# Optimization experiments

Measured on AMD Instinct MI355X. Metric: run time of the kernel, lower is better.

## Reference

```python
import jax, jax.numpy as jnp
import numpy as np

B, T, EMB, H = 4, 2048, 1024, 16
S = EMB // H


def setup_inputs() -> dict:
    key = jax.random.key(0)
    ks = jax.random.split(key, 7)
    x = jax.random.normal(ks[0], (B, T, EMB), dtype=jnp.float32)
    pad_amounts = jax.random.randint(ks[1], (B,), 0, 512, dtype=jnp.int64)
    Wk = jax.random.normal(ks[2], (S, S), dtype=jnp.float32) * (1.0 / np.sqrt(S))
    Wq = jax.random.normal(ks[3], (S, S), dtype=jnp.float32) * (1.0 / np.sqrt(S))
    Wv = jax.random.normal(ks[4], (S, S), dtype=jnp.float32) * (1.0 / np.sqrt(S))
    Wu = jax.random.normal(ks[5], (EMB, EMB), dtype=jnp.float32) * (1.0 / np.sqrt(EMB))
    bu = jax.random.normal(ks[6], (EMB,), dtype=jnp.float32) * 0.01
    return {"x": x, "Wk": Wk, "Wq": Wq, "Wv": Wv, "Wu": Wu, "bu": bu,
            "pad_amounts": pad_amounts}


def reference(x, Wk, Wq, Wv, Wu, bu, pad_amounts):
    b, t, e = x.shape
    h = H
    s = e // h
    xh = x.reshape(b, t, h, s)
    # torch Linear: y = x @ W.T (no bias for k/q/v)
    keys = jnp.einsum('bths,os->btho', xh, Wk)
    queries = jnp.einsum('bths,os->btho', xh, Wq)
    values = jnp.einsum('bths,os->btho', xh, Wv)
    # (b,t,h,s) -> (b*h,t,s)
    keys = keys.transpose(0, 2, 1, 3).reshape(b * h, t, s)
    queries = queries.transpose(0, 2, 1, 3).reshape(b * h, t, s)
    values = values.transpose(0, 2, 1, 3).reshape(b * h, t, s)
    scale = e ** 0.25
    queries = queries / scale
    keys = keys / scale
    dot = jnp.einsum('nqs,nks->nqk', queries, keys)  # (b*h, t, t)
    # Faithful to original bug: only the first b flat indices of b*h get masked.
    pad_full = jnp.concatenate([pad_amounts,
                                jnp.zeros(b * h - b, dtype=pad_amounts.dtype)])
    thresh = (t - pad_full)[:, None, None]  # (b*h,1,1); thresh=t -> no mask
    pos = jnp.arange(t)
    mask = (pos[None, :, None] >= thresh) & (pos[None, None, :] >= thresh)
    dot = jnp.where(mask, -jnp.inf, dot)
    att = jax.nn.softmax(dot, axis=2)
    out = jnp.einsum('nqk,nks->nqs', att, values)  # (b*h,t,s)
    out = out.reshape(b, h, t, s).transpose(0, 2, 1, 3).reshape(b, t, h * s)
    return out @ Wu.T + bu
```

## Files before the change

### kernel.cpp

```cpp
#include <hip/hip_runtime.h>


typedef float f32x4 __attribute__((ext_vector_type(4)));
typedef float f32x16 __attribute__((ext_vector_type(16)));
typedef _Float16 f16x2 __attribute__((ext_vector_type(2)));
typedef _Float16 f16x8 __attribute__((ext_vector_type(8)));
typedef unsigned u32x4 __attribute__((ext_vector_type(4)));

#define MFMA16(a, b, c) __builtin_amdgcn_mfma_f32_16x16x32_f16((a), (b), (c), 0, 0, 0)
#define MFMA32(a, b, c) __builtin_amdgcn_mfma_f32_32x32x16_f16((a), (b), (c), 0, 0, 0)

constexpr int Tn = 2048;
constexpr int Bn = 4;
constexpr int EMBn = 1024;
constexpr float NEG_INF = -3.0e38f;

__device__ __forceinline__ float exp2_hw(float x) {
  float r; asm("v_exp_f32 %0, %1" : "=v"(r) : "v"(x)); return r;
}
__device__ __forceinline__ unsigned pkrtz(float lo, float hi) {
  unsigned r; asm("v_cvt_pkrtz_f16_f32 %0, %1, %2" : "=v"(r) : "v"(lo), "v"(hi)); return r;
}
__device__ __forceinline__ unsigned pkadd(unsigned a, unsigned b) {
  unsigned r; asm("v_pk_add_f16 %0, %1, %2" : "=v"(r) : "v"(a), "v"(b)); return r;
}
__device__ __forceinline__ void permswap(unsigned& a, unsigned& b) {
  asm("v_permlane32_swap_b32 %0, %1" : "+v"(a), "+v"(b));
}

__global__ __launch_bounds__(256) void sa_prep(
    const float* __restrict__ Wk, const float* __restrict__ Wq,
    const float* __restrict__ Wv, const float* __restrict__ Wu,
    _Float16* __restrict__ w3, _Float16* __restrict__ wub) {
  int idx = blockIdx.x * 256 + threadIdx.x;
  const float rs = 0.21233046f;
  if (idx < 1048576) wub[idx] = (_Float16)Wu[idx];
  if (idx < 4096) {
    w3[idx]        = (_Float16)(Wk[idx] * rs);
    w3[4096 + idx] = (_Float16)(Wq[idx] * rs);
    w3[8192 + idx] = (_Float16)(Wv[idx]);
  }
}

__global__ __launch_bounds__(256) void sa_qkv(
    const float* __restrict__ x, const _Float16* __restrict__ w3,
    _Float16* __restrict__ Qb, _Float16* __restrict__ Kb, _Float16* __restrict__ Vt) {
  const int wave = threadIdx.x >> 6;
  const int lane = threadIdx.x & 63;
  const int g = lane >> 4, c = lane & 15;
  const int n = blockIdx.y, b = n >> 4, h = n & 15;
  const int t0 = blockIdx.x * 64 + wave * 16;

  f16x8 ax[2];
#pragma unroll
  for (int kk = 0; kk < 2; ++kk) {
    const float* xp = x + ((long)((b * Tn + t0 + c) * 16 + h)) * 64 + kk * 32 + g * 8;
    f32x4 u = *(const f32x4*)xp;
    f32x4 v = *(const f32x4*)(xp + 4);
    f16x8 a;
    a[0] = (_Float16)u[0]; a[1] = (_Float16)u[1]; a[2] = (_Float16)u[2]; a[3] = (_Float16)u[3];
    a[4] = (_Float16)v[0]; a[5] = (_Float16)v[1]; a[6] = (_Float16)v[2]; a[7] = (_Float16)v[3];
    ax[kk] = a;
  }

#pragma unroll
  for (int w = 0; w < 2; ++w) {
    _Float16* dst = w ? Qb : Kb;
#pragma unroll
    for (int ot = 0; ot < 4; ++ot) {
      f32x4 a_ = {0.f, 0.f, 0.f, 0.f};
#pragma unroll
      for (int kk = 0; kk < 2; ++kk) {
        f16x8 wf = *(const f16x8*)(w3 + w * 4096 + (ot * 16 + c) * 64 + kk * 32 + g * 8);
        a_ = MFMA16(ax[kk], wf, a_);
      }
#pragma unroll
      for (int r = 0; r < 4; ++r)
        dst[((long)n * Tn + t0 + g * 4 + r) * 64 + ot * 16 + c] = (_Float16)a_[r];
    }
  }

#pragma unroll
  for (int ot = 0; ot < 4; ++ot) {
    f32x4 a_ = {0.f, 0.f, 0.f, 0.f};
#pragma unroll
    for (int kk = 0; kk < 2; ++kk) {
      f16x8 wf = *(const f16x8*)(w3 + 8192 + (ot * 16 + c) * 64 + kk * 32 + g * 8);
      a_ = MFMA16(wf, ax[kk], a_);
    }
#pragma unroll
    for (int r = 0; r < 4; ++r)
      Vt[((long)n * 64 + ot * 16 + g * 4 + r) * Tn + t0 + c] = (_Float16)a_[r];
  }
}

__global__ __launch_bounds__(256, 4) void sa_flash(
    const _Float16* __restrict__ Qb, const _Float16* __restrict__ Kb,
    const _Float16* __restrict__ Vt, const int* __restrict__ pad32,
    _Float16* __restrict__ AO) {
  const int bid = blockIdx.x;
  const int n = (bid & 7) * 8 + (bid >> 7);
  const int qblk = (bid >> 3) & 15;
  const int tid = threadIdx.x;
  const int wave = tid >> 6;
  const int lane = tid & 63;
  const int ql = lane & 31;
  const int hi = lane >> 5;

  int thresh = Tn;
  if (n < Bn) {
    bool is64 = (pad32[1] == 0 && pad32[3] == 0);
    int pv = is64 ? pad32[2 * n] : pad32[n];
    thresh = Tn - pv;
  }

  const int qbase = qblk * 128 + wave * 32;
  const _Float16* Qh = Qb + (long)n * Tn * 64;
  const _Float16* Kh = Kb + (long)n * Tn * 64;
  const _Float16* Vh = Vt + (long)n * 64 * Tn;

  f16x8 bq[4];
  const _Float16* qp = Qh + (long)(qbase + ql) * 64 + hi * 8;
#pragma unroll
  for (int ks = 0; ks < 4; ++ks) bq[ks] = *(const f16x8*)(qp + ks * 16);

  __shared__ __align__(16) char smem[36864];

  const int sr = tid >> 2, sc = tid & 3;
  const _Float16* kgp = Kh + sr * 64 + sc * 8;
  const _Float16* vgp = Vh + (long)sr * Tn + sc * 8;
  char* kw = smem + sr * 144 + sc * 16;
  char* vw = smem + 18432 + sr * 144 + sc * 16;

  f32x16 o[2];
  f32x16 zf;
#pragma unroll
  for (int i = 0; i < 16; ++i) { o[0][i] = 0.f; o[1][i] = 0.f; zf[i] = 0.f; }
  float l = 0.f;

  const bool qge = (qbase + ql) >= thresh;
  const bool qany = (qbase + 32) > thresh;

  {
    f16x8 k0 = *(const f16x8*)kgp;
    f16x8 k1 = *(const f16x8*)(kgp + 32);
    f16x8 v0 = *(const f16x8*)vgp;
    f16x8 v1 = *(const f16x8*)(vgp + 32);
    *(f16x8*)kw = k0;
    *(f16x8*)(kw + 64) = k1;
    *(f16x8*)vw = v0;
    *(f16x8*)(vw + 64) = v1;
  }
  __syncthreads();

  int cur = 0;
  for (int kb = 0; kb < Tn; kb += 64) {
    const int kbn = (kb + 64) & (Tn - 1);
    f16x8 kst0 = *(const f16x8*)(kgp + kbn * 64);
    f16x8 kst1 = *(const f16x8*)(kgp + kbn * 64 + 32);
    f16x8 vst0 = *(const f16x8*)(vgp + kbn);
    f16x8 vst1 = *(const f16x8*)(vgp + kbn + 32);

    const char* kbb = smem + cur * 9216;
    const char* vbb = smem + 18432 + cur * 9216;

#pragma unroll
    for (int sub = 0; sub < 2; ++sub) {
      const char* krow = kbb + (sub * 32 + ql) * 144 + hi * 16;
      f16x8 ka0 = *(const f16x8*)(krow);
      f16x8 ka1 = *(const f16x8*)(krow + 32);
      f16x8 ka2 = *(const f16x8*)(krow + 64);
      f16x8 ka3 = *(const f16x8*)(krow + 96);

      __builtin_amdgcn_s_setprio(1);
      f32x16 st = MFMA32(ka0, bq[0], zf);
      st = MFMA32(ka1, bq[1], st);
      st = MFMA32(ka2, bq[2], st);
      st = MFMA32(ka3, bq[3], st);
      __builtin_amdgcn_s_setprio(0);

      if (qany && (kb + sub * 32 + 32) > thresh) {
        if (qge) {
#pragma unroll
          for (int r = 0; r < 16; ++r) {
            int kr_ = kb + sub * 32 + (r & 3) + 8 * (r >> 2) + 4 * hi;
            if (kr_ >= thresh) st[r] = NEG_INF;
          }
        }
      }

      float p[16];
#pragma unroll
      for (int r = 0; r < 16; ++r) p[r] = exp2_hw(st[r]);

      unsigned pw[8], psum[2];
#pragma unroll
      for (int j = 0; j < 2; ++j) {
        unsigned a0 = pkrtz(p[j * 8 + 0], p[j * 8 + 1]);
        unsigned b0 = pkrtz(p[j * 8 + 4], p[j * 8 + 5]);
        unsigned a1 = pkrtz(p[j * 8 + 2], p[j * 8 + 3]);
        unsigned b1 = pkrtz(p[j * 8 + 6], p[j * 8 + 7]);
        psum[j] = pkadd(pkadd(a0, b0), pkadd(a1, b1));
        permswap(a0, b0);
        permswap(a1, b1);
        pw[j * 4 + 0] = a0; pw[j * 4 + 1] = a1;
        pw[j * 4 + 2] = b0; pw[j * 4 + 3] = b1;
      }
      {
        f16x2 ph = __builtin_bit_cast(f16x2, pkadd(psum[0], psum[1]));
        l += (float)ph[0] + (float)ph[1];
      }
      u32x4 u0 = {pw[0], pw[1], pw[2], pw[3]};
      u32x4 u1 = {pw[4], pw[5], pw[6], pw[7]};
      f16x8 pb0 = __builtin_bit_cast(f16x8, u0);
      f16x8 pb1 = __builtin_bit_cast(f16x8, u1);

      const char* vrow0 = vbb + ql * 144 + sub * 64 + hi * 16;
      const char* vrow1 = vrow0 + 32 * 144;
      f16x8 va0 = *(const f16x8*)(vrow0);
      f16x8 va1 = *(const f16x8*)(vrow0 + 32);
      f16x8 va2 = *(const f16x8*)(vrow1);
      f16x8 va3 = *(const f16x8*)(vrow1 + 32);

      __builtin_amdgcn_s_setprio(1);
      o[0] = MFMA32(va0, pb0, o[0]);
      o[0] = MFMA32(va1, pb1, o[0]);
      o[1] = MFMA32(va2, pb0, o[1]);
      o[1] = MFMA32(va3, pb1, o[1]);
      __builtin_amdgcn_s_setprio(0);
    }

    char* kwd = kw + (cur ^ 1) * 9216;
    char* vwd = vw + (cur ^ 1) * 9216;
    *(f16x8*)kwd = kst0;
    *(f16x8*)(kwd + 64) = kst1;
    *(f16x8*)vwd = vst0;
    *(f16x8*)(vwd + 64) = vst1;
    __syncthreads();
    cur ^= 1;
  }

  float lf = l + __shfl_xor(l, 32, 64);
  float linv = 1.0f / lf;

  _Float16* my = (_Float16*)(smem + wave * 4096);
#pragma unroll
  for (int stile = 0; stile < 2; ++stile) {
#pragma unroll
    for (int r = 0; r < 16; r += 2) {
      unsigned wv = pkrtz(o[stile][r] * linv, o[stile][r + 1] * linv);
      int s = stile * 32 + (r & 3) + 8 * (r >> 2) + 4 * hi;
      *(unsigned*)(my + ql * 64 + (s ^ ((ql & 7) << 3))) = wv;
    }
  }
  asm volatile("s_waitcnt lgkmcnt(0)" ::: "memory");

  const int bb = n >> 4, hh = n & 15;
  const int qr = lane >> 3, s0 = (lane & 7) * 8;
#pragma unroll
  for (int j = 0; j < 4; ++j) {
    int q = j * 8 + qr;
    f16x8 vv = *(const f16x8*)(my + q * 64 + (s0 ^ ((q & 7) << 3)));
    *(f16x8*)(AO + ((long)(bb * Tn + qbase + q)) * EMBn + hh * 64 + s0) = vv;
  }
}

__global__ __launch_bounds__(256, 4) void sa_oproj(
    const _Float16* __restrict__ A, const _Float16* __restrict__ WuB,
    const float* __restrict__ bu, float* __restrict__ Y) {
  const int bid = blockIdx.x;
  const int xcd = bid & 7;
  const int j = bid >> 3;
  const int nstrip = j & 15;
  const int mblk = xcd * 8 + (j >> 4);
  const int tid = threadIdx.x;
  const int wave = tid >> 6;
  const int lane = tid & 63;
  const int ql = lane & 31;
  const int hi = lane >> 5;
  const int mbase = mblk * 128 + wave * 32;
  const int nbase = nstrip * 64;

  __shared__ __align__(16) char bsm[18432];
  const int sr = tid >> 3, sc = tid & 7;
  const _Float16* wg0 = WuB + (long)(nbase + sr) * 1024 + sc * 8;
  const _Float16* wg1 = WuB + (long)(nbase + sr + 32) * 1024 + sc * 8;
  char* ww0 = bsm + sr * 144 + sc * 16;
  char* ww1 = bsm + (sr + 32) * 144 + sc * 16;

  const _Float16* ap = A + (long)(mbase + ql) * 1024 + hi * 8;

  f32x16 acc[2];
#pragma unroll
  for (int i = 0; i < 16; ++i) { acc[0][i] = 0.f; acc[1][i] = 0.f; }

  {
    f16x8 w0 = *(const f16x8*)wg0;
    f16x8 w1 = *(const f16x8*)wg1;
    *(f16x8*)ww0 = w0;
    *(f16x8*)ww1 = w1;
  }
  __syncthreads();

  int cur = 0;
  for (int kb = 0; kb < 1024; kb += 64) {
    const int kbn = (kb + 64) & 1023;
    f16x8 wn0 = *(const f16x8*)(wg0 + kbn);
    f16x8 wn1 = *(const f16x8*)(wg1 + kbn);

    f16x8 af[4];
#pragma unroll
    for (int ks = 0; ks < 4; ++ks) af[ks] = *(const f16x8*)(ap + kb + ks * 16);

    const char* bbase = bsm + cur * 9216;
#pragma unroll
    for (int nt = 0; nt < 2; ++nt) {
      const char* brow = bbase + (nt * 32 + ql) * 144;
#pragma unroll
      for (int ks = 0; ks < 4; ++ks) {
        f16x8 bf = *(const f16x8*)(brow + (ks * 2 + hi) * 16);
        acc[nt] = MFMA32(af[ks], bf, acc[nt]);
      }
    }

    *(f16x8*)(ww0 + (cur ^ 1) * 9216) = wn0;
    *(f16x8*)(ww1 + (cur ^ 1) * 9216) = wn1;
    __syncthreads();
    cur ^= 1;
  }

#pragma unroll
  for (int nt = 0; nt < 2; ++nt) {
    float bias = bu[nbase + nt * 32 + ql];
#pragma unroll
    for (int r = 0; r < 16; ++r) {
      int mrow = mbase + (r & 3) + 8 * (r >> 2) + 4 * hi;
      Y[(long)mrow * 1024 + nbase + nt * 32 + ql] = acc[nt][r] + bias;
    }
  }
}

extern "C" void kernel_launch(void* const* d_in, const int* in_sizes, int n_in,
                              void* d_out, int out_size, void* d_ws, size_t ws_size,
                              hipStream_t stream) {
  const float* x  = (const float*)d_in[0];
  const float* Wk = (const float*)d_in[1];
  const float* Wq = (const float*)d_in[2];
  const float* Wv = (const float*)d_in[3];
  const float* Wu = (const float*)d_in[4];
  const float* bu = (const float*)d_in[5];
  const int* pad  = (const int*)d_in[6];
  float* Y = (float*)d_out;

  _Float16* ws  = (_Float16*)d_ws;
  _Float16* w3  = ws;
  _Float16* wub = ws + 16384;
  _Float16* Qb  = ws + 16384 + 1048576;
  _Float16* Kb  = Qb + 8388608;
  _Float16* Vt  = Kb + 8388608;
  _Float16* AO  = Vt + 8388608;

  sa_prep<<<4096, 256, 0, stream>>>(Wk, Wq, Wv, Wu, w3, wub);
  sa_qkv<<<dim3(32, 64), 256, 0, stream>>>(x, w3, Qb, Kb, Vt);
  sa_flash<<<dim3(1024), 256, 0, stream>>>(Qb, Kb, Vt, pad, AO);
  sa_oproj<<<dim3(1024), 256, 0, stream>>>(AO, wub, bu, Y);
}
```

Before: 153.0 us.

## Fuse Wu fp16 conversion into out-projection and split QK/softmax phases

Removes the separate pass that converts the 1024x1024 Wu matrix to fp16 in the prep kernel. The out-projection kernel now loads fp32 Wu tiles and converts them to fp16 in registers before writing to LDS, and the prep launch shrinks to 16 blocks. Separately, the flash kernel computes both 32-row QK^T sub-tiles before running exp/softmax on either, to give the scheduler more independent MFMA work. The cost is twice the global bytes for Wu reads in oproj, repeated across blocks, plus higher register pressure in the flash loop.

```diff
diff --git a/kernel.cpp b/kernel.cpp
--- a/kernel.cpp
+++ b/kernel.cpp
@@ -30,11 +30,9 @@
 
 __global__ __launch_bounds__(256) void sa_prep(
     const float* __restrict__ Wk, const float* __restrict__ Wq,
-    const float* __restrict__ Wv, const float* __restrict__ Wu,
-    _Float16* __restrict__ w3, _Float16* __restrict__ wub) {
+    const float* __restrict__ Wv, _Float16* __restrict__ w3) {
   int idx = blockIdx.x * 256 + threadIdx.x;
   const float rs = 0.21233046f;
-  if (idx < 1048576) wub[idx] = (_Float16)Wu[idx];
   if (idx < 4096) {
     w3[idx]        = (_Float16)(Wk[idx] * rs);
     w3[4096 + idx] = (_Float16)(Wq[idx] * rs);
@@ -164,6 +162,7 @@
     const char* kbb = smem + cur * 9216;
     const char* vbb = smem + 18432 + cur * 9216;
 
+    f32x16 st[2];
 #pragma unroll
     for (int sub = 0; sub < 2; ++sub) {
       const char* krow = kbb + (sub * 32 + ql) * 144 + hi * 16;
@@ -171,12 +170,11 @@
       f16x8 ka1 = *(const f16x8*)(krow + 32);
       f16x8 ka2 = *(const f16x8*)(krow + 64);
       f16x8 ka3 = *(const f16x8*)(krow + 96);
-
       __builtin_amdgcn_s_setprio(1);
-      f32x16 st = MFMA32(ka0, bq[0], zf);
-      st = MFMA32(ka1, bq[1], st);
-      st = MFMA32(ka2, bq[2], st);
-      st = MFMA32(ka3, bq[3], st);
+      f32x16 s_ = MFMA32(ka0, bq[0], zf);
+      s_ = MFMA32(ka1, bq[1], s_);
+      s_ = MFMA32(ka2, bq[2], s_);
+      s_ = MFMA32(ka3, bq[3], s_);
       __builtin_amdgcn_s_setprio(0);
 
       if (qany && (kb + sub * 32 + 32) > thresh) {
@@ -184,14 +182,18 @@
 #pragma unroll
           for (int r = 0; r < 16; ++r) {
             int kr_ = kb + sub * 32 + (r & 3) + 8 * (r >> 2) + 4 * hi;
-            if (kr_ >= thresh) st[r] = NEG_INF;
+            if (kr_ >= thresh) s_[r] = NEG_INF;
           }
         }
       }
-
+      st[sub] = s_;
+    }
+
+#pragma unroll
+    for (int sub = 0; sub < 2; ++sub) {
       float p[16];
 #pragma unroll
-      for (int r = 0; r < 16; ++r) p[r] = exp2_hw(st[r]);
+      for (int r = 0; r < 16; ++r) p[r] = exp2_hw(st[sub][r]);
 
       unsigned pw[8], psum[2];
 #pragma unroll
@@ -266,7 +268,7 @@
 }
 
 __global__ __launch_bounds__(256, 4) void sa_oproj(
-    const _Float16* __restrict__ A, const _Float16* __restrict__ WuB,
+    const _Float16* __restrict__ A, const float* __restrict__ Wu,
     const float* __restrict__ bu, float* __restrict__ Y) {
   const int bid = blockIdx.x;
   const int xcd = bid & 7;
@@ -283,8 +285,8 @@
 
   __shared__ __align__(16) char bsm[18432];
   const int sr = tid >> 3, sc = tid & 7;
-  const _Float16* wg0 = WuB + (long)(nbase + sr) * 1024 + sc * 8;
-  const _Float16* wg1 = WuB + (long)(nbase + sr + 32) * 1024 + sc * 8;
+  const float* wg0 = Wu + (long)(nbase + sr) * 1024 + sc * 8;
+  const float* wg1 = Wu + (long)(nbase + sr + 32) * 1024 + sc * 8;
   char* ww0 = bsm + sr * 144 + sc * 16;
   char* ww1 = bsm + (sr + 32) * 144 + sc * 16;
 
@@ -294,9 +296,21 @@
 #pragma unroll
   for (int i = 0; i < 16; ++i) { acc[0][i] = 0.f; acc[1][i] = 0.f; }
 
+  auto cvt8 = [](const float* p) -> f16x8 {
+    f32x4 a = *(const f32x4*)p;
+    f32x4 b = *(const f32x4*)(p + 4);
+    unsigned r0, r1, r2, r3;
+    asm("v_cvt_pkrtz_f16_f32 %0, %1, %2" : "=v"(r0) : "v"(a[0]), "v"(a[1]));
+    asm("v_cvt_pkrtz_f16_f32 %0, %1, %2" : "=v"(r1) : "v"(a[2]), "v"(a[3]));
+    asm("v_cvt_pkrtz_f16_f32 %0, %1, %2" : "=v"(r2) : "v"(b[0]), "v"(b[1]));
+    asm("v_cvt_pkrtz_f16_f32 %0, %1, %2" : "=v"(r3) : "v"(b[2]), "v"(b[3]));
+    u32x4 u = {r0, r1, r2, r3};
+    return __builtin_bit_cast(f16x8, u);
+  };
+
   {
-    f16x8 w0 = *(const f16x8*)wg0;
-    f16x8 w1 = *(const f16x8*)wg1;
+    f16x8 w0 = cvt8(wg0);
+    f16x8 w1 = cvt8(wg1);
     *(f16x8*)ww0 = w0;
     *(f16x8*)ww1 = w1;
   }
@@ -305,8 +319,8 @@
   int cur = 0;
   for (int kb = 0; kb < 1024; kb += 64) {
     const int kbn = (kb + 64) & 1023;
-    f16x8 wn0 = *(const f16x8*)(wg0 + kbn);
-    f16x8 wn1 = *(const f16x8*)(wg1 + kbn);
+    f16x8 wn0 = cvt8(wg0 + kbn);
+    f16x8 wn1 = cvt8(wg1 + kbn);
 
     f16x8 af[4];
 #pragma unroll
@@ -354,14 +368,13 @@
 
   _Float16* ws  = (_Float16*)d_ws;
   _Float16* w3  = ws;
-  _Float16* wub = ws + 16384;
-  _Float16* Qb  = ws + 16384 + 1048576;
+  _Float16* Qb  = ws + 16384;
   _Float16* Kb  = Qb + 8388608;
   _Float16* Vt  = Kb + 8388608;
   _Float16* AO  = Vt + 8388608;
 
-  sa_prep<<<4096, 256, 0, stream>>>(Wk, Wq, Wv, Wu, w3, wub);
+  sa_prep<<<16, 256, 0, stream>>>(Wk, Wq, Wv, w3);
   sa_qkv<<<dim3(32, 64), 256, 0, stream>>>(x, w3, Qb, Kb, Vt);
   sa_flash<<<dim3(1024), 256, 0, stream>>>(Qb, Kb, Vt, pad, AO);
-  sa_oproj<<<dim3(1024), 256, 0, stream>>>(AO, wub, bu, Y);
-}
+  sa_oproj<<<dim3(1024), 256, 0, stream>>>(AO, Wu, bu, Y);
+}
```

After: 165.9 us. 1.08x slower.

## Process two 32-row query tiles per wave in flash attention kernel

Applied to the files above, without the earlier changes.

Each wave now handles 64 query rows instead of 32, so each block covers 256 queries and the grid shrinks from 1024 to 512 blocks. Every K/V tile staged in shared memory is reused for twice as many query rows, which halves global K/V traffic and LDS loads per query. The cost is more accumulator registers (launch bounds lowered to 2 blocks per SM) and fewer blocks in flight, which may reduce latency hiding across the 256 CUs.

```diff
diff --git a/kernel.cpp b/kernel.cpp
--- a/kernel.cpp
+++ b/kernel.cpp
@@ -94,13 +94,13 @@
   }
 }
 
-__global__ __launch_bounds__(256, 4) void sa_flash(
+__global__ __launch_bounds__(256, 2) void sa_flash(
     const _Float16* __restrict__ Qb, const _Float16* __restrict__ Kb,
     const _Float16* __restrict__ Vt, const int* __restrict__ pad32,
     _Float16* __restrict__ AO) {
   const int bid = blockIdx.x;
-  const int n = (bid & 7) * 8 + (bid >> 7);
-  const int qblk = (bid >> 3) & 15;
+  const int n = (bid & 7) * 8 + (bid >> 6);
+  const int qblk = (bid >> 3) & 7;
   const int tid = threadIdx.x;
   const int wave = tid >> 6;
   const int lane = tid & 63;
@@ -114,15 +114,18 @@
     thresh = Tn - pv;
   }
 
-  const int qbase = qblk * 128 + wave * 32;
+  const int qbase = qblk * 256 + wave * 64;
   const _Float16* Qh = Qb + (long)n * Tn * 64;
   const _Float16* Kh = Kb + (long)n * Tn * 64;
   const _Float16* Vh = Vt + (long)n * 64 * Tn;
 
-  f16x8 bq[4];
-  const _Float16* qp = Qh + (long)(qbase + ql) * 64 + hi * 8;
-#pragma unroll
-  for (int ks = 0; ks < 4; ++ks) bq[ks] = *(const f16x8*)(qp + ks * 16);
+  f16x8 bq[2][4];
+#pragma unroll
+  for (int qh = 0; qh < 2; ++qh) {
+    const _Float16* qp = Qh + (long)(qbase + qh * 32 + ql) * 64 + hi * 8;
+#pragma unroll
+    for (int ks = 0; ks < 4; ++ks) bq[qh][ks] = *(const f16x8*)(qp + ks * 16);
+  }
 
   __shared__ __align__(16) char smem[36864];
 
@@ -132,14 +135,18 @@
   char* kw = smem + sr * 144 + sc * 16;
   char* vw = smem + 18432 + sr * 144 + sc * 16;
 
-  f32x16 o[2];
+  f32x16 o[2][2];
   f32x16 zf;
 #pragma unroll
-  for (int i = 0; i < 16; ++i) { o[0][i] = 0.f; o[1][i] = 0.f; zf[i] = 0.f; }
-  float l = 0.f;
-
-  const bool qge = (qbase + ql) >= thresh;
-  const bool qany = (qbase + 32) > thresh;
+  for (int i = 0; i < 16; ++i) {
+    o[0][0][i] = 0.f; o[0][1][i] = 0.f; o[1][0][i] = 0.f; o[1][1][i] = 0.f;
+    zf[i] = 0.f;
+  }
+  float l0 = 0.f, l1 = 0.f;
+
+  const bool qge0 = (qbase + ql) >= thresh;
+  const bool qge1 = (qbase + 32 + ql) >= thresh;
+  const bool qany = (qbase + 64) > thresh;
 
   {
     f16x8 k0 = *(const f16x8*)kgp;
@@ -173,47 +180,26 @@
       f16x8 ka3 = *(const f16x8*)(krow + 96);
 
       __builtin_amdgcn_s_setprio(1);
-      f32x16 st = MFMA32(ka0, bq[0], zf);
-      st = MFMA32(ka1, bq[1], st);
-      st = MFMA32(ka2, bq[2], st);
-      st = MFMA32(ka3, bq[3], st);
+      f32x16 st0 = MFMA32(ka0, bq[0][0], zf);
+      f32x16 st1 = MFMA32(ka0, bq[1][0], zf);
+      st0 = MFMA32(ka1, bq[0][1], st0);
+      st1 = MFMA32(ka1, bq[1][1], st1);
+      st0 = MFMA32(ka2, bq[0][2], st0);
+      st1 = MFMA32(ka2, bq[1][2], st1);
+      st0 = MFMA32(ka3, bq[0][3], st0);
+      st1 = MFMA32(ka3, bq[1][3], st1);
       __builtin_amdgcn_s_setprio(0);
 
       if (qany && (kb + sub * 32 + 32) > thresh) {
-        if (qge) {
-#pragma unroll
-          for (int r = 0; r < 16; ++r) {
-            int kr_ = kb + sub * 32 + (r & 3) + 8 * (r >> 2) + 4 * hi;
-            if (kr_ >= thresh) st[r] = NEG_INF;
+#pragma unroll
+        for (int r = 0; r < 16; ++r) {
+          int kr_ = kb + sub * 32 + (r & 3) + 8 * (r >> 2) + 4 * hi;
+          if (kr_ >= thresh) {
+            if (qge0) st0[r] = NEG_INF;
+            if (qge1) st1[r] = NEG_INF;
           }
         }
       }
-
-      float p[16];
-#pragma unroll
-      for (int r = 0; r < 16; ++r) p[r] = exp2_hw(st[r]);
-
-      unsigned pw[8], psum[2];
-#pragma unroll
-      for (int j = 0; j < 2; ++j) {
-        unsigned a0 = pkrtz(p[j * 8 + 0], p[j * 8 + 1]);
-        unsigned b0 = pkrtz(p[j * 8 + 4], p[j * 8 + 5]);
-        unsigned a1 = pkrtz(p[j * 8 + 2], p[j * 8 + 3]);
-        unsigned b1 = pkrtz(p[j * 8 + 6], p[j * 8 + 7]);
-        psum[j] = pkadd(pkadd(a0, b0), pkadd(a1, b1));
-        permswap(a0, b0);
-        permswap(a1, b1);
-        pw[j * 4 + 0] = a0; pw[j * 4 + 1] = a1;
-        pw[j * 4 + 2] = b0; pw[j * 4 + 3] = b1;
-      }
-      {
-        f16x2 ph = __builtin_bit_cast(f16x2, pkadd(psum[0], psum[1]));
-        l += (float)ph[0] + (float)ph[1];
-      }
-      u32x4 u0 = {pw[0], pw[1], pw[2], pw[3]};
-      u32x4 u1 = {pw[4], pw[5], pw[6], pw[7]};
-      f16x8 pb0 = __builtin_bit_cast(f16x8, u0);
-      f16x8 pb1 = __builtin_bit_cast(f16x8, u1);
 
       const char* vrow0 = vbb + ql * 144 + sub * 64 + hi * 16;
       const char* vrow1 = vrow0 + 32 * 144;
@@ -222,12 +208,43 @@
       f16x8 va2 = *(const f16x8*)(vrow1);
       f16x8 va3 = *(const f16x8*)(vrow1 + 32);
 
-      __builtin_amdgcn_s_setprio(1);
-      o[0] = MFMA32(va0, pb0, o[0]);
-      o[0] = MFMA32(va1, pb1, o[0]);
-      o[1] = MFMA32(va2, pb0, o[1]);
-      o[1] = MFMA32(va3, pb1, o[1]);
-      __builtin_amdgcn_s_setprio(0);
+#pragma unroll
+      for (int qh = 0; qh < 2; ++qh) {
+        const f32x16& stq = qh ? st1 : st0;
+        float p[16];
+#pragma unroll
+        for (int r = 0; r < 16; ++r) p[r] = exp2_hw(stq[r]);
+
+        unsigned pw[8], psum[2];
+#pragma unroll
+        for (int j = 0; j < 2; ++j) {
+          unsigned a0 = pkrtz(p[j * 8 + 0], p[j * 8 + 1]);
+          unsigned b0 = pkrtz(p[j * 8 + 4], p[j * 8 + 5]);
+          unsigned a1 = pkrtz(p[j * 8 + 2], p[j * 8 + 3]);
+          unsigned b1 = pkrtz(p[j * 8 + 6], p[j * 8 + 7]);
+          psum[j] = pkadd(pkadd(a0, b0), pkadd(a1, b1));
+          permswap(a0, b0);
+          permswap(a1, b1);
+          pw[j * 4 + 0] = a0; pw[j * 4 + 1] = a1;
+          pw[j * 4 + 2] = b0; pw[j * 4 + 3] = b1;
+        }
+        {
+          f16x2 ph = __builtin_bit_cast(f16x2, pkadd(psum[0], psum[1]));
+          if (qh) l1 += (float)ph[0] + (float)ph[1];
+          else    l0 += (float)ph[0] + (float)ph[1];
+        }
+        u32x4 u0 = {pw[0], pw[1], pw[2], pw[3]};
+        u32x4 u1 = {pw[4], pw[5], pw[6], pw[7]};
+        f16x8 pb0 = __builtin_bit_cast(f16x8, u0);
+        f16x8 pb1 = __builtin_bit_cast(f16x8, u1);
+
+        __builtin_amdgcn_s_setprio(1);
+        o[qh][0] = MFMA32(va0, pb0, o[qh][0]);
+        o[qh][0] = MFMA32(va1, pb1, o[qh][0]);
+        o[qh][1] = MFMA32(va2, pb0, o[qh][1]);
+        o[qh][1] = MFMA32(va3, pb1, o[qh][1]);
+        __builtin_amdgcn_s_setprio(0);
+      }
     }
 
     char* kwd = kw + (cur ^ 1) * 9216;
@@ -240,28 +257,39 @@
     cur ^= 1;
   }
 
-  float lf = l + __shfl_xor(l, 32, 64);
-  float linv = 1.0f / lf;
-
-  _Float16* my = (_Float16*)(smem + wave * 4096);
-#pragma unroll
-  for (int stile = 0; stile < 2; ++stile) {
-#pragma unroll
-    for (int r = 0; r < 16; r += 2) {
-      unsigned wv = pkrtz(o[stile][r] * linv, o[stile][r + 1] * linv);
-      int s = stile * 32 + (r & 3) + 8 * (r >> 2) + 4 * hi;
-      *(unsigned*)(my + ql * 64 + (s ^ ((ql & 7) << 3))) = wv;
-    }
-  }
-  asm volatile("s_waitcnt lgkmcnt(0)" ::: "memory");
+  float lf0 = l0 + __shfl_xor(l0, 32, 64);
+  float lf1 = l1 + __shfl_xor(l1, 32, 64);
+  float linv0 = 1.0f / lf0;
+  float linv1 = 1.0f / lf1;
 
   const int bb = n >> 4, hh = n & 15;
   const int qr = lane >> 3, s0 = (lane & 7) * 8;
-#pragma unroll
-  for (int j = 0; j < 4; ++j) {
-    int q = j * 8 + qr;
-    f16x8 vv = *(const f16x8*)(my + q * 64 + (s0 ^ ((q & 7) << 3)));
-    *(f16x8*)(AO + ((long)(bb * Tn + qbase + q)) * EMBn + hh * 64 + s0) = vv;
+  _Float16* my = (_Float16*)(smem + wave * 8192);
+#pragma unroll
+  for (int qh = 0; qh < 2; ++qh) {
+    float linv = qh ? linv1 : linv0;
+    _Float16* myq = my + qh * 2048;
+#pragma unroll
+    for (int stile = 0; stile < 2; ++stile) {
+#pragma unroll
+      for (int r = 0; r < 16; r += 2) {
+        unsigned wv = pkrtz(o[qh][stile][r] * linv, o[qh][stile][r + 1] * linv);
+        int s = stile * 32 + (r & 3) + 8 * (r >> 2) + 4 * hi;
+        *(unsigned*)(myq + ql * 64 + (s ^ ((ql & 7) << 3))) = wv;
+      }
+    }
+  }
+  asm volatile("s_waitcnt lgkmcnt(0)" ::: "memory");
+
+#pragma unroll
+  for (int qh = 0; qh < 2; ++qh) {
+    _Float16* myq = my + qh * 2048;
+#pragma unroll
+    for (int j = 0; j < 4; ++j) {
+      int q = j * 8 + qr;
+      f16x8 vv = *(const f16x8*)(myq + q * 64 + (s0 ^ ((q & 7) << 3)));
+      *(f16x8*)(AO + ((long)(bb * Tn + qbase + qh * 32 + q)) * EMBn + hh * 64 + s0) = vv;
+    }
   }
 }
 
@@ -362,6 +390,6 @@
 
   sa_prep<<<4096, 256, 0, stream>>>(Wk, Wq, Wv, Wu, w3, wub);
   sa_qkv<<<dim3(32, 64), 256, 0, stream>>>(x, w3, Qb, Kb, Vt);
-  sa_flash<<<dim3(1024), 256, 0, stream>>>(Qb, Kb, Vt, pad, AO);
+  sa_flash<<<dim3(512), 256, 0, stream>>>(Qb, Kb, Vt, pad, AO);
   sa_oproj<<<dim3(1024), 256, 0, stream>>>(AO, wub, bu, Y);
 }
```

Measured after the change: 148.0 us. 3.3% less time.
